# Performance work log

Measured on AMD Instinct MI355X. Metric: run time of the kernel, lower is better.

Reference implementation:

```python
import jax, jax.numpy as jnp
import numpy as np

GROUP_SIZE = 128
EPS = 1e-8


def _quantize_ste(weight, scale, group_size=GROUP_SIZE):
    """Binary {-1,+1} group-scaled quantization with straight-through estimator."""
    shape = weight.shape
    flat = weight.reshape(-1)
    n = flat.shape[0]
    pad = (-n) % group_size
    if pad:
        flat = jnp.pad(flat, (0, pad))
    groups = flat.reshape(-1, group_size)              # [n_groups, g]
    s = jnp.maximum(jnp.abs(scale[: groups.shape[0]]), EPS)[:, None]
    normalized = groups / s
    smooth = jnp.tanh(normalized)
    hard = jnp.sign(normalized)
    hard = jnp.where(hard == 0, jnp.ones_like(hard), hard)
    # STE: forward value is `hard`, gradient flows through tanh
    binary_w = jax.lax.stop_gradient(hard) + smooth - jax.lax.stop_gradient(smooth)
    quantized = binary_w * s
    return quantized.reshape(-1)[:n].reshape(shape)


def setup_inputs() -> dict:
    key = jax.random.key(0)
    k1, k2, k3, k4 = jax.random.split(key, 4)
    B, S, IN, OUT = 4, 2048, 4096, 11008
    n_groups = (OUT * IN + GROUP_SIZE - 1) // GROUP_SIZE  # 352256
    x = jax.random.normal(k1, (B, S, IN), dtype=jnp.float32)
    weight = jax.random.normal(k2, (OUT, IN), dtype=jnp.float32) * 0.02
    bias = jax.random.normal(k3, (OUT,), dtype=jnp.float32) * 0.01
    scale = jax.random.uniform(k4, (n_groups,), dtype=jnp.float32, minval=0.01, maxval=1.0)
    return {"x": x, "weight": weight, "bias": bias, "scale": scale}


def reference(x, weight, bias, scale):
    w_bin = _quantize_ste(weight, scale)               # [OUT, IN]
    # F.linear: y = x @ w_bin.T + bias
    return jnp.einsum("bsi,oi->bso", x, w_bin) + bias
```

## Files before the change

### kernel.cpp

```cpp
#include <hip/hip_runtime.h>
#include <hip/hip_bf16.h>
#include <stdint.h>

#define IN_DIM   4096
#define OUT_DIM  11008
#define M_DIM    8192

typedef unsigned short u16;
typedef __bf16 bf16_t;
typedef bf16_t bf16x8 __attribute__((ext_vector_type(8)));
typedef float  f32x4  __attribute__((ext_vector_type(4)));
typedef u16    u16x8  __attribute__((ext_vector_type(8)));

static __device__ __forceinline__ u16 f2bf(float f) {
    __bf16 h = (__bf16)f;
    return __builtin_bit_cast(unsigned short, h);
}

static __device__ __forceinline__ void async_copy16(void* lds_uniform, const void* gaddr) {
    __builtin_amdgcn_global_load_lds(
        (const __attribute__((address_space(1))) uint32_t*)(uintptr_t)gaddr,
        (__attribute__((address_space(3))) uint32_t*)(uintptr_t)lds_uniform,
        16, 0, 0);
}

#define XB_BLOCKS ((M_DIM * IN_DIM / 8) / 256)
#define WB_BLOCKS ((OUT_DIM * IN_DIM / 8) / 256)

__global__ void prep_kernel(const float* __restrict__ x, const float* __restrict__ w,
                            const float* __restrict__ scale,
                            u16x8* __restrict__ xb, u16x8* __restrict__ wb) {
    if (blockIdx.x < XB_BLOCKS) {
        int i = blockIdx.x * 256 + threadIdx.x;
        const float4* p = (const float4*)x + 2 * (size_t)i;
        float4 a = p[0];
        float4 b = p[1];
        u16x8 r;
        r[0] = f2bf(a.x); r[1] = f2bf(a.y); r[2] = f2bf(a.z); r[3] = f2bf(a.w);
        r[4] = f2bf(b.x); r[5] = f2bf(b.y); r[6] = f2bf(b.z); r[7] = f2bf(b.w);
        xb[i] = r;
    } else {
        int i = (blockIdx.x - XB_BLOCKS) * 256 + threadIdx.x;
        int g = i >> 4;
        float s = fmaxf(fabsf(scale[g]), 1e-8f);
        u16 bs = f2bf(s);
        const float4* p = (const float4*)w + 2 * (size_t)i;
        float4 a = p[0];
        float4 b = p[1];
        u16x8 r;
        r[0] = bs | ((a.x < 0.f) ? 0x8000 : 0);
        r[1] = bs | ((a.y < 0.f) ? 0x8000 : 0);
        r[2] = bs | ((a.z < 0.f) ? 0x8000 : 0);
        r[3] = bs | ((a.w < 0.f) ? 0x8000 : 0);
        r[4] = bs | ((b.x < 0.f) ? 0x8000 : 0);
        r[5] = bs | ((b.y < 0.f) ? 0x8000 : 0);
        r[6] = bs | ((b.z < 0.f) ? 0x8000 : 0);
        r[7] = bs | ((b.w < 0.f) ? 0x8000 : 0);
        wb[i] = r;
    }
}


#define BM 256
#define BN 256
#define NPID_M (M_DIM / BM)
#define NPID_N (OUT_DIM / BN)

#define BAR()        __builtin_amdgcn_s_barrier()
#define WAIT_VM(n)   asm volatile("s_waitcnt vmcnt(" #n ")" ::: "memory")
#define WAIT_LGKM(n) asm volatile("s_waitcnt lgkmcnt(" #n ")" ::: "memory")
#define PRIO(p)      __builtin_amdgcn_s_setprio(p)
#define SCHEDB()     __builtin_amdgcn_sched_barrier(0)

#define STG_A(b, j, kt) async_copy16(&sA[b][((j)*64 + wid*8) * 64], \
                                     gA + (size_t)(j) * 64 * IN_DIM + ((kt) & 63) * 64)
#define STG_B(b, j, kt) async_copy16(&sB[b][((j)*64 + wid*8) * 64], \
                                     gB + (size_t)(j) * 64 * IN_DIM + ((kt) & 63) * 64)
#define STAGE_A(b, h, kt) do { STG_A(b, 2*(h), kt); STG_A(b, 2*(h)+1, kt); } while (0)
#define STAGE_B(b, h, kt) do { STG_B(b, 2*(h), kt); STG_B(b, 2*(h)+1, kt); } while (0)

#define LDA(b, mh) do {                                                   \
    _Pragma("unroll")                                                     \
    for (int m_ = 0; m_ < 4; ++m_) {                                      \
      const int r_ = arb + ((mh)*4 + m_) * 16;                            \
      aF[m_][0] = *(const bf16x8*)&sA[b][r_ * 64 + sw0];                  \
      aF[m_][1] = *(const bf16x8*)&sA[b][r_ * 64 + sw1];                  \
    }                                                                     \
  } while (0)

#define LDB(b, nh, BF) do {                                               \
    _Pragma("unroll")                                                     \
    for (int n_ = 0; n_ < 2; ++n_) {                                      \
      const int r_ = brb + ((nh)*2 + n_) * 16;                            \
      BF[n_][0] = *(const bf16x8*)&sB[b][r_ * 64 + sw0];                  \
      BF[n_][1] = *(const bf16x8*)&sB[b][r_ * 64 + sw1];                  \
    }                                                                     \
  } while (0)

#define MFMA_Q(mh, BF, nh) do {                                           \
    _Pragma("unroll")                                                     \
    for (int ks_ = 0; ks_ < 2; ++ks_)                                     \
      _Pragma("unroll")                                                   \
      for (int m_ = 0; m_ < 4; ++m_)                                      \
        _Pragma("unroll")                                                 \
        for (int n_ = 0; n_ < 2; ++n_)                                    \
          acc[(mh)*4 + m_][(nh)*2 + n_] =                                 \
              __builtin_amdgcn_mfma_f32_16x16x32_bf16(                    \
                  aF[m_][ks_], BF[n_][ks_],                               \
                  acc[(mh)*4 + m_][(nh)*2 + n_], 0, 0, 0);                \
  } while (0)

#define PH_TOP() do { BAR(); WAIT_LGKM(0); SCHEDB(); PRIO(1); } while (0)
#define PH_END() do { PRIO(0); BAR(); } while (0)

__global__ __launch_bounds__(512, 2) void gemm_kernel(const u16* __restrict__ A,
                                                      const u16* __restrict__ Bw,
                                                      const float* __restrict__ bias,
                                                      float* __restrict__ out) {
    __shared__ __align__(16) u16 sA[2][BM * 64];
    __shared__ __align__(16) u16 sB[2][BN * 64];

    const int pid0  = blockIdx.x;
    const int pid   = (pid0 & 7) * (NPID_M * NPID_N / 8) + (pid0 >> 3);
    const int pid_m = pid / NPID_N;
    const int pid_n = pid - pid_m * NPID_N;
    const int m0 = pid_m * BM;
    const int n0 = pid_n * BN;

    const int tid  = threadIdx.x;
    const int wid  = tid >> 6;
    const int lane = tid & 63;
    const int wm   = (wid >> 2) * 128;
    const int wn   = (wid & 3) * 64;

    const int lrow = lane >> 3;
    const int gc   = (lane & 7) ^ lrow;
    const u16* gA = A  + (size_t)(m0 + wid * 8 + lrow) * IN_DIM + gc * 8;
    const u16* gB = Bw + (size_t)(n0 + wid * 8 + lrow) * IN_DIM + gc * 8;

    const int row16 = lane & 15;
    const int quad  = lane >> 4;
    const int arb   = wm + row16;
    const int brb   = wn + row16;
    const int sw0   = ((0 * 4 + quad) ^ (row16 & 7)) * 8;
    const int sw1   = ((1 * 4 + quad) ^ (row16 & 7)) * 8;

    f32x4 acc[8][4];
#pragma unroll
    for (int mt = 0; mt < 8; ++mt)
#pragma unroll
        for (int nt = 0; nt < 4; ++nt)
            acc[mt][nt] = (f32x4){0.f, 0.f, 0.f, 0.f};

    bf16x8 aF[4][2], bF0[2][2], bF1[2][2];

    STAGE_A(0, 0, 0); STAGE_A(0, 1, 0);
    STAGE_B(0, 0, 0); STAGE_B(0, 1, 0);
    STAGE_B(1, 0, 1); STAGE_A(1, 0, 1);
    WAIT_VM(4);
    BAR();

    for (int i = 0; i < IN_DIM / 128; ++i) {
        const int kt = 2 * i;
        LDA(0, 0); LDB(0, 0, bF0);
        STAGE_A(1, 1, kt + 1);
        WAIT_LGKM(8);
        PH_TOP(); MFMA_Q(0, bF0, 0); PH_END();
        LDB(0, 1, bF1);
        STAGE_B(1, 1, kt + 1);
        PH_TOP(); MFMA_Q(0, bF1, 1); PH_END();
        LDA(0, 1);
        STAGE_B(0, 0, kt + 2);
        PH_TOP(); MFMA_Q(1, bF0, 0); PH_END();
        STAGE_A(0, 0, kt + 2);
        BAR(); WAIT_LGKM(0); SCHEDB(); PRIO(1);
        MFMA_Q(1, bF1, 1);
        PRIO(0); WAIT_VM(4); BAR();
        LDA(1, 0); LDB(1, 0, bF0);
        STAGE_A(0, 1, kt + 2);
        WAIT_LGKM(8);
        PH_TOP(); MFMA_Q(0, bF0, 0); PH_END();
        LDB(1, 1, bF1);
        STAGE_B(0, 1, kt + 2);
        PH_TOP(); MFMA_Q(0, bF1, 1); PH_END();
        LDA(1, 1);
        STAGE_B(1, 0, kt + 3);
        PH_TOP(); MFMA_Q(1, bF0, 0); PH_END();
        STAGE_A(1, 0, kt + 3);
        BAR(); WAIT_LGKM(0); SCHEDB(); PRIO(1);
        MFMA_Q(1, bF1, 1);
        PRIO(0); WAIT_VM(4); BAR();
    }
    WAIT_VM(0);

#pragma unroll
    for (int nt = 0; nt < 4; ++nt) {
        int col  = n0 + wn + nt * 16 + row16;
        float bv = bias[col];
#pragma unroll
        for (int mt = 0; mt < 8; ++mt) {
            int row = m0 + wm + mt * 16 + quad * 4;
            float* po = out + (size_t)row * OUT_DIM + col;
#pragma unroll
            for (int r = 0; r < 4; ++r)
                __builtin_nontemporal_store(acc[mt][nt][r] + bv, po + (size_t)r * OUT_DIM);
        }
    }
}

__global__ void naive_kernel(const float* __restrict__ x, const float* __restrict__ wt,
                             const float* __restrict__ bias, const float* __restrict__ scale,
                             float* __restrict__ out) {
    long idx = (long)blockIdx.x * 256 + threadIdx.x;
    if (idx >= (long)M_DIM * OUT_DIM) return;
    int m = (int)(idx / OUT_DIM);
    int o = (int)(idx % OUT_DIM);
    const float* xr = x + (size_t)m * IN_DIM;
    const float* wr = wt + (size_t)o * IN_DIM;
    float acc = 0.f;
    for (int gb = 0; gb < IN_DIM / 128; ++gb) {
        float s = fmaxf(fabsf(scale[o * (IN_DIM / 128) + gb]), 1e-8f);
        float part = 0.f;
        for (int k = 0; k < 128; ++k) {
            float wv = wr[gb * 128 + k];
            part += (wv >= 0.f) ? xr[gb * 128 + k] : -xr[gb * 128 + k];
        }
        acc += part * s;
    }
    out[idx] = acc + bias[o];
}

extern "C" void kernel_launch(void* const* d_in, const int* in_sizes, int n_in,
                              void* d_out, int out_size, void* d_ws, size_t ws_size,
                              hipStream_t stream) {
    const float* x     = (const float*)d_in[0];
    const float* wt    = (const float*)d_in[1];
    const float* bias  = (const float*)d_in[2];
    const float* scale = (const float*)d_in[3];
    float* out = (float*)d_out;

    const size_t xb_bytes = (size_t)M_DIM * IN_DIM * sizeof(u16);
    const size_t wb_bytes = (size_t)OUT_DIM * IN_DIM * sizeof(u16);

    if (ws_size >= xb_bytes + wb_bytes) {
        u16* xb = (u16*)d_ws;
        u16* wb = (u16*)((char*)d_ws + xb_bytes);

        prep_kernel<<<XB_BLOCKS + WB_BLOCKS, 256, 0, stream>>>(
            x, wt, scale, (u16x8*)xb, (u16x8*)wb);

        gemm_kernel<<<NPID_M * NPID_N, 512, 0, stream>>>(xb, wb, bias, out);
    } else {
        long total = (long)M_DIM * OUT_DIM;
        int blocks = (int)((total + 255) / 256);
        naive_kernel<<<blocks, 256, 0, stream>>>(x, wt, bias, scale, out);
    }
}
```

Before: 1.136 ms.

## Rework GEMM LDS staging schedule and use grid-stride prep with nontemporal loads

Restructures the GEMM main loop so both LDS buffers are fully prefetched up front, with stage loads issued in quarter-tile chunks that match each MFMA phase. Fewer barriers sit around each MFMA block, and B rows are remapped so each wave's staged rows line up with the quarter being consumed. The prep kernel becomes a grid-stride loop over a fixed block count and uses nontemporal loads for the fp32 inputs. The gain is meant to come from better overlap of global-to-LDS traffic with MFMA work and lower launch and cache overhead in prep. The risk is more complex vmcnt/barrier correctness and possible LDS hazards.

```diff
diff --git a/kernel.cpp b/kernel.cpp
--- a/kernel.cpp
+++ b/kernel.cpp
@@ -24,39 +24,43 @@
         16, 0, 0);
 }
 
-#define XB_BLOCKS ((M_DIM * IN_DIM / 8) / 256)
-#define WB_BLOCKS ((OUT_DIM * IN_DIM / 8) / 256)
-
-__global__ void prep_kernel(const float* __restrict__ x, const float* __restrict__ w,
-                            const float* __restrict__ scale,
-                            u16x8* __restrict__ xb, u16x8* __restrict__ wb) {
-    if (blockIdx.x < XB_BLOCKS) {
-        int i = blockIdx.x * 256 + threadIdx.x;
-        const float4* p = (const float4*)x + 2 * (size_t)i;
-        float4 a = p[0];
-        float4 b = p[1];
-        u16x8 r;
-        r[0] = f2bf(a.x); r[1] = f2bf(a.y); r[2] = f2bf(a.z); r[3] = f2bf(a.w);
-        r[4] = f2bf(b.x); r[5] = f2bf(b.y); r[6] = f2bf(b.z); r[7] = f2bf(b.w);
-        xb[i] = r;
-    } else {
-        int i = (blockIdx.x - XB_BLOCKS) * 256 + threadIdx.x;
-        int g = i >> 4;
-        float s = fmaxf(fabsf(scale[g]), 1e-8f);
-        u16 bs = f2bf(s);
-        const float4* p = (const float4*)w + 2 * (size_t)i;
-        float4 a = p[0];
-        float4 b = p[1];
-        u16x8 r;
-        r[0] = bs | ((a.x < 0.f) ? 0x8000 : 0);
-        r[1] = bs | ((a.y < 0.f) ? 0x8000 : 0);
-        r[2] = bs | ((a.z < 0.f) ? 0x8000 : 0);
-        r[3] = bs | ((a.w < 0.f) ? 0x8000 : 0);
-        r[4] = bs | ((b.x < 0.f) ? 0x8000 : 0);
-        r[5] = bs | ((b.y < 0.f) ? 0x8000 : 0);
-        r[6] = bs | ((b.z < 0.f) ? 0x8000 : 0);
-        r[7] = bs | ((b.w < 0.f) ? 0x8000 : 0);
-        wb[i] = r;
+#define PREP_BLOCKS 4096
+
+__global__ __launch_bounds__(256) void prep_kernel(const float* __restrict__ x,
+                                                   const float* __restrict__ w,
+                                                   const float* __restrict__ scale,
+                                                   u16x8* __restrict__ xb,
+                                                   u16x8* __restrict__ wb) {
+    const int XB_UNITS  = M_DIM * IN_DIM / 8;
+    const int TOT_UNITS = XB_UNITS + OUT_DIM * IN_DIM / 8;
+    for (int u = blockIdx.x * 256 + threadIdx.x; u < TOT_UNITS; u += PREP_BLOCKS * 256) {
+        if (u < XB_UNITS) {
+            const f32x4* p = (const f32x4*)x + 2 * (size_t)u;
+            f32x4 a = __builtin_nontemporal_load(p);
+            f32x4 b = __builtin_nontemporal_load(p + 1);
+            u16x8 r;
+            r[0] = f2bf(a[0]); r[1] = f2bf(a[1]); r[2] = f2bf(a[2]); r[3] = f2bf(a[3]);
+            r[4] = f2bf(b[0]); r[5] = f2bf(b[1]); r[6] = f2bf(b[2]); r[7] = f2bf(b[3]);
+            xb[u] = r;
+        } else {
+            int i = u - XB_UNITS;
+            int g = i >> 4;
+            float s = fmaxf(fabsf(scale[g]), 1e-8f);
+            u16 bs = f2bf(s);
+            const f32x4* p = (const f32x4*)w + 2 * (size_t)i;
+            f32x4 a = __builtin_nontemporal_load(p);
+            f32x4 b = __builtin_nontemporal_load(p + 1);
+            u16x8 r;
+            r[0] = bs | ((a[0] < 0.f) ? 0x8000 : 0);
+            r[1] = bs | ((a[1] < 0.f) ? 0x8000 : 0);
+            r[2] = bs | ((a[2] < 0.f) ? 0x8000 : 0);
+            r[3] = bs | ((a[3] < 0.f) ? 0x8000 : 0);
+            r[4] = bs | ((b[0] < 0.f) ? 0x8000 : 0);
+            r[5] = bs | ((b[1] < 0.f) ? 0x8000 : 0);
+            r[6] = bs | ((b[2] < 0.f) ? 0x8000 : 0);
+            r[7] = bs | ((b[3] < 0.f) ? 0x8000 : 0);
+            wb[i] = r;
+        }
     }
 }
 
@@ -74,10 +78,14 @@
 
 #define STG_A(b, j, kt) async_copy16(&sA[b][((j)*64 + wid*8) * 64], \
                                      gA + (size_t)(j) * 64 * IN_DIM + ((kt) & 63) * 64)
-#define STG_B(b, j, kt) async_copy16(&sB[b][((j)*64 + wid*8) * 64], \
-                                     gB + (size_t)(j) * 64 * IN_DIM + ((kt) & 63) * 64)
-#define STAGE_A(b, h, kt) do { STG_A(b, 2*(h), kt); STG_A(b, 2*(h)+1, kt); } while (0)
-#define STAGE_B(b, h, kt) do { STG_B(b, 2*(h), kt); STG_B(b, 2*(h)+1, kt); } while (0)
+#define ROWB0(j) (((j) >> 1) * 128 + ((j) & 1) * 32)
+#define STG_B(b, j, kt) async_copy16(&sB[b][(ROWB0(j) + (wid>>2)*64 + (wid&3)*8) * 64], \
+                                     gB + (size_t)ROWB0(j) * IN_DIM + ((kt) & 63) * 64)
+
+#define STAGE_A02(b, kt) do { STG_A(b, 0, kt); STG_A(b, 2, kt); } while (0)
+#define STAGE_A13(b, kt) do { STG_A(b, 1, kt); STG_A(b, 3, kt); } while (0)
+#define STAGE_B02(b, kt) do { STG_B(b, 0, kt); STG_B(b, 2, kt); } while (0)
+#define STAGE_B13(b, kt) do { STG_B(b, 1, kt); STG_B(b, 3, kt); } while (0)
 
 #define LDA(b, mh) do {                                                   \
     _Pragma("unroll")                                                     \
@@ -110,8 +118,10 @@
                   acc[(mh)*4 + m_][(nh)*2 + n_], 0, 0, 0);                \
   } while (0)
 
-#define PH_TOP() do { BAR(); WAIT_LGKM(0); SCHEDB(); PRIO(1); } while (0)
-#define PH_END() do { PRIO(0); BAR(); } while (0)
+#define MFMA_TOP(mh, BF, nh) do {                                         \
+    WAIT_LGKM(0); SCHEDB();                                               \
+    PRIO(1); MFMA_Q(mh, BF, nh); PRIO(0); SCHEDB();                       \
+  } while (0)
 
 __global__ __launch_bounds__(512, 2) void gemm_kernel(const u16* __restrict__ A,
                                                       const u16* __restrict__ Bw,
@@ -136,7 +146,7 @@
     const int lrow = lane >> 3;
     const int gc   = (lane & 7) ^ lrow;
     const u16* gA = A  + (size_t)(m0 + wid * 8 + lrow) * IN_DIM + gc * 8;
-    const u16* gB = Bw + (size_t)(n0 + wid * 8 + lrow) * IN_DIM + gc * 8;
+    const u16* gB = Bw + (size_t)(n0 + (wid >> 2) * 64 + (wid & 3) * 8 + lrow) * IN_DIM + gc * 8;
 
     const int row16 = lane & 15;
     const int quad  = lane >> 4;
@@ -154,44 +164,39 @@
 
     bf16x8 aF[4][2], bF0[2][2], bF1[2][2];
 
-    STAGE_A(0, 0, 0); STAGE_A(0, 1, 0);
-    STAGE_B(0, 0, 0); STAGE_B(0, 1, 0);
-    STAGE_B(1, 0, 1); STAGE_A(1, 0, 1);
-    WAIT_VM(4);
+    STAGE_A02(0, 0); STAGE_B02(0, 0); STAGE_B13(0, 0); STAGE_A13(0, 0);
+    STAGE_A02(1, 1); STAGE_B02(1, 1); STAGE_B13(1, 1); STAGE_A13(1, 1);
+    WAIT_VM(10);
     BAR();
+    LDA(0, 0); LDB(0, 0, bF0);
 
     for (int i = 0; i < IN_DIM / 128; ++i) {
         const int kt = 2 * i;
+        MFMA_TOP(0, bF0, 0);
+        LDB(0, 1, bF1);
+        STAGE_A02(0, kt + 2); WAIT_VM(10); BAR();
+        MFMA_TOP(0, bF1, 1);
+        LDA(0, 1);
+        STAGE_B02(0, kt + 2); BAR();
+        MFMA_TOP(1, bF0, 0);
+        STAGE_B13(0, kt + 2); WAIT_VM(10); BAR();
+        MFMA_TOP(1, bF1, 1);
+        LDA(1, 0); LDB(1, 0, bF0);
+        STAGE_A13(0, kt + 2); WAIT_VM(10); BAR();
+        MFMA_TOP(0, bF0, 0);
+        LDB(1, 1, bF1);
+        STAGE_A02(1, kt + 3); WAIT_VM(10); BAR();
+        MFMA_TOP(0, bF1, 1);
+        LDA(1, 1);
+        STAGE_B02(1, kt + 3); BAR();
+        MFMA_TOP(1, bF0, 0);
+        STAGE_B13(1, kt + 3); WAIT_VM(10); BAR();
+        MFMA_TOP(1, bF1, 1);
         LDA(0, 0); LDB(0, 0, bF0);
-        STAGE_A(1, 1, kt + 1);
-        WAIT_LGKM(8);
-        PH_TOP(); MFMA_Q(0, bF0, 0); PH_END();
-        LDB(0, 1, bF1);
-        STAGE_B(1, 1, kt + 1);
-        PH_TOP(); MFMA_Q(0, bF1, 1); PH_END();
-        LDA(0, 1);
-        STAGE_B(0, 0, kt + 2);
-        PH_TOP(); MFMA_Q(1, bF0, 0); PH_END();
-        STAGE_A(0, 0, kt + 2);
-        BAR(); WAIT_LGKM(0); SCHEDB(); PRIO(1);
-        MFMA_Q(1, bF1, 1);
-        PRIO(0); WAIT_VM(4); BAR();
-        LDA(1, 0); LDB(1, 0, bF0);
-        STAGE_A(0, 1, kt + 2);
-        WAIT_LGKM(8);
-        PH_TOP(); MFMA_Q(0, bF0, 0); PH_END();
-        LDB(1, 1, bF1);
-        STAGE_B(0, 1, kt + 2);
-        PH_TOP(); MFMA_Q(0, bF1, 1); PH_END();
-        LDA(1, 1);
-        STAGE_B(1, 0, kt + 3);
-        PH_TOP(); MFMA_Q(1, bF0, 0); PH_END();
-        STAGE_A(1, 0, kt + 3);
-        BAR(); WAIT_LGKM(0); SCHEDB(); PRIO(1);
-        MFMA_Q(1, bF1, 1);
-        PRIO(0); WAIT_VM(4); BAR();
+        STAGE_A13(1, kt + 3); WAIT_VM(10); BAR();
     }
     WAIT_VM(0);
+    WAIT_LGKM(0);
 
 #pragma unroll
     for (int nt = 0; nt < 4; ++nt) {
@@ -246,7 +251,7 @@
         u16* xb = (u16*)d_ws;
         u16* wb = (u16*)((char*)d_ws + xb_bytes);
 
-        prep_kernel<<<XB_BLOCKS + WB_BLOCKS, 256, 0, stream>>>(
+        prep_kernel<<<PREP_BLOCKS, 256, 0, stream>>>(
             x, wt, scale, (u16x8*)xb, (u16x8*)wb);
 
         gemm_kernel<<<NPID_M * NPID_N, 512, 0, stream>>>(xb, wb, bias, out);
```

New measurement: 1.084 ms. -4.6%, faster.
